# Performance work log

Hardware: AMD Instinct MI355X
Metric: run time of the kernel (lower is better)

Reference implementation:

```python
import jax, jax.numpy as jnp
import numpy as np

WINDOW = 5  # window_size from init
C_COARSE = 256
C_FINE = 128


def _gather_windows(fine_nchw, b, lin_idx, stride, pad, w, wc):
    """Extract [M, w*w, C] windows centered on coarse grid cells.

    Equivalent to F.unfold(kernel=w, stride=stride, padding=pad) followed by
    rearrange('n (c ww) l -> n l ww c') and fancy-indexing [b, lin_idx],
    but gathers only the matched windows.
    """
    x = jnp.pad(fine_nchw, ((0, 0), (0, 0), (pad, pad), (pad, pad)))
    x = jnp.transpose(x, (0, 2, 3, 1))  # [N, Hp, Wp, C]
    r = lin_idx // wc
    c = lin_idx % wc
    offs = jnp.arange(w)
    rows = r[:, None] * stride + offs  # [M, w] (start = r*stride - pad, +pad shift)
    cols = c[:, None] * stride + offs  # [M, w]
    patches = x[b[:, None, None], rows[:, :, None], cols[:, None, :]]  # [M, w, w, C]
    return patches.reshape(patches.shape[0], w * w, patches.shape[-1])


def setup_inputs() -> dict:
    key = jax.random.key(0)
    ks = jax.random.split(key, 10)
    N, Hc, Hf, M = 2, 60, 240, 3000
    inp = {
        "coarse_image_feature_1": jax.random.normal(ks[0], (N, Hc * Hc, C_COARSE), jnp.float32),
        "coarse_image_feature_2": jax.random.normal(ks[1], (N, Hc * Hc, C_COARSE), jnp.float32),
        "fine_image_feature_1": jax.random.normal(ks[2], (N, C_FINE, Hf, Hf), jnp.float32),
        "fine_image_feature_2": jax.random.normal(ks[3], (N, C_FINE, Hf, Hf), jnp.float32),
        "batch_indices": jax.random.randint(ks[4], (M,), 0, N),
        "row_indices": jax.random.randint(ks[5], (M,), 0, Hc * Hc),
        "column_indices": jax.random.randint(ks[6], (M,), 0, Hc * Hc),
        "fine_height_width": Hf,
        "coarse_height_width": Hc,
        # learned params (kaiming-normal-ish weights, zero biases)
        "W_dp": jax.random.normal(ks[7], (C_FINE, C_COARSE), jnp.float32) * np.sqrt(2.0 / C_FINE),
        "b_dp": jnp.zeros((C_FINE,), jnp.float32),
        "W_merge": jax.random.normal(ks[8], (C_FINE, 2 * C_FINE), jnp.float32) * np.sqrt(2.0 / C_FINE),
        "b_merge": jnp.zeros((C_FINE,), jnp.float32),
    }
    return inp


def reference(coarse_image_feature_1, coarse_image_feature_2,
              fine_image_feature_1, fine_image_feature_2,
              batch_indices, row_indices, column_indices,
              fine_height_width, coarse_height_width,
              W_dp, b_dp, W_merge, b_merge):
    stride = fine_height_width // coarse_height_width
    pad = WINDOW // 2
    M = batch_indices.shape[0]

    f1 = _gather_windows(fine_image_feature_1, batch_indices, row_indices,
                         stride, pad, WINDOW, coarse_height_width)       # [M, ww, Cf]
    f2 = _gather_windows(fine_image_feature_2, batch_indices, column_indices,
                         stride, pad, WINDOW, coarse_height_width)       # [M, ww, Cf]

    coarse = jnp.concatenate([
        coarse_image_feature_1[batch_indices, row_indices],
        coarse_image_feature_2[batch_indices, column_indices],
    ], axis=0)                                                           # [2M, Cc]
    coarse = coarse @ W_dp.T + b_dp                                      # [2M, Cf]

    fine = jnp.concatenate([f1, f2], axis=0)                             # [2M, ww, Cf]
    combined = jnp.concatenate(
        [fine, jnp.broadcast_to(coarse[:, None, :], fine.shape)], axis=-1)  # [2M, ww, 2Cf]
    merged = combined @ W_merge.T + b_merge                              # [2M, ww, Cf]
    return merged[:M], merged[M:]
```

## Files before the change

### kernel.cpp

```cpp
#include <hip/hip_runtime.h>

#define HF 240
#define HC 60
#define STRIDEF 4
#define PADW 2
#define WIN 5
#define CC 256
#define CF 128
#define NPOS 25
#define NPX (HF*HF)
#define MPB 16

typedef __bf16 bf16x8 __attribute__((ext_vector_type(8)));
typedef __bf16 bf16x4 __attribute__((ext_vector_type(4)));
typedef float  f32x4  __attribute__((ext_vector_type(4)));

__global__ void k_prep(const float* __restrict__ W_dp, const float* __restrict__ b_dp,
                       const float* __restrict__ W_merge, const float* __restrict__ b_merge,
                       __bf16* __restrict__ Wm1h, float* __restrict__ W_effT,
                       float* __restrict__ b_eff) {
    const int j = blockIdx.x;
    const int k = threadIdx.x;
    const float* wm2 = W_merge + (size_t)j * (2 * CF) + CF;

    float acc = 0.f, accb = 0.f;
    for (int q = 0; q < CF; ++q) {
        const float wq = wm2[q];
        acc  += wq * W_dp[(size_t)q * CC + k];
        accb += wq * b_dp[q];
    }
    W_effT[(size_t)k * CF + j] = acc;

    if (k < CF)
        Wm1h[(size_t)j * CF + k] = (__bf16)W_merge[(size_t)j * (2 * CF) + k];
    if (k == 0)
        b_eff[j] = accb + b_merge[j];
}

__global__ void k_coarse(const float* __restrict__ c1, const float* __restrict__ c2,
                         const int* __restrict__ bidx, const int* __restrict__ ridx,
                         const int* __restrict__ cidx, int M,
                         const float* __restrict__ W_effT, const float* __restrict__ b_eff,
                         float* __restrict__ c_all) {
    const int m0 = blockIdx.x * MPB;
    const int j  = threadIdx.x;
    const int twoM = 2 * M;
    __shared__ float v[MPB * CC];

    const int nm = (twoM - m0) < MPB ? (twoM - m0) : MPB;
    for (int mm = 0; mm < nm; ++mm) {
        int m = m0 + mm;
        const float* src;
        if (m < M) src = c1 + ((size_t)bidx[m] * (HC * HC) + ridx[m]) * CC;
        else       src = c2 + ((size_t)bidx[m - M] * (HC * HC) + cidx[m - M]) * CC;
        v[mm * CC + j]      = src[j];
        v[mm * CC + j + CF] = src[j + CF];
    }
    __syncthreads();

    float acc[MPB];
    const float be = b_eff[j];
    #pragma unroll
    for (int mm = 0; mm < MPB; ++mm) acc[mm] = be;

    for (int k = 0; k < CC; k += 4) {
        float w0 = W_effT[(k + 0) * CF + j];
        float w1 = W_effT[(k + 1) * CF + j];
        float w2 = W_effT[(k + 2) * CF + j];
        float w3 = W_effT[(k + 3) * CF + j];
        #pragma unroll
        for (int mm = 0; mm < MPB; ++mm) {
            const f32x4 vv = *(const f32x4*)&v[mm * CC + k];
            acc[mm] += w0 * vv.x + w1 * vv.y + w2 * vv.z + w3 * vv.w;
        }
    }
    for (int mm = 0; mm < nm; ++mm)
        c_all[(size_t)(m0 + mm) * CF + j] = acc[mm];
}

__global__ __launch_bounds__(256) void k_transpose(
    const float* __restrict__ f1, const float* __restrict__ f2,
    __bf16* __restrict__ T) {
    const int slot = blockIdx.y;
    const float* src = (slot >= 2 ? f2 : f1) + (size_t)(slot & 1) * CF * NPX;
    const int px0 = blockIdx.x * 64;
    const int t = threadIdx.x;

    __shared__ __bf16 tile[64 * CF];

    const int px_l  = t & 63;
    const int chseg = t >> 6;
    const int sw = (px_l & 15) << 3;
    const float* colp = src + px0 + px_l;
    #pragma unroll
    for (int q = 0; q < 8; ++q) {
        const int ch0 = chseg * 32 + q * 4;
        const float v0 = colp[(size_t)(ch0 + 0) * NPX];
        const float v1 = colp[(size_t)(ch0 + 1) * NPX];
        const float v2 = colp[(size_t)(ch0 + 2) * NPX];
        const float v3 = colp[(size_t)(ch0 + 3) * NPX];
        bf16x4 pk = { (__bf16)v0, (__bf16)v1, (__bf16)v2, (__bf16)v3 };
        *(bf16x4*)&tile[px_l * CF + (ch0 ^ sw)] = pk;
    }
    __syncthreads();

    const int l = t & 63;
    const int w = t >> 6;
    __bf16* dst = T + ((size_t)slot * NPX + px0) * CF;
    #pragma unroll
    for (int i = 0; i < 4; ++i) {
        const int pr  = w * 16 + i * 4 + (l >> 4);
        const int ch0 = (l & 15) * 8;
        const bf16x8 vv = *(const bf16x8*)&tile[pr * CF + (ch0 ^ ((pr & 15) << 3))];
        *(bf16x8*)&dst[(size_t)pr * CF + ch0] = vv;
    }
}

__global__ __launch_bounds__(256) void k_main(
    const __bf16* __restrict__ T,
    const int* __restrict__ bidx, const int* __restrict__ ridx,
    const int* __restrict__ cidx, int M,
    const __bf16* __restrict__ Wm1h, const float* __restrict__ c_all,
    float* __restrict__ out) {

    const int m = blockIdx.x;
    const int t = threadIdx.x;
    const int l    = t & 63;
    const int wv   = t >> 6;
    const int lo16 = l & 15;
    const int hi   = l >> 4;

    __shared__ uint patchU[32 * 64];
    __bf16* patch = (__bf16*)patchU;

    int b, lin, ii;
    if (m < M) { ii = 0; b = bidx[m];     lin = ridx[m]; }
    else       { ii = 1; b = bidx[m - M]; lin = cidx[m - M]; }
    const int slot = ii * 2 + b;
    const int r  = lin / HC, c = lin - r * HC;
    const int y0 = r * STRIDEF - PADW;
    const int x0 = c * STRIDEF - PADW;

    bf16x8 bfrag[2][4];
    #pragma unroll
    for (int nt2 = 0; nt2 < 2; ++nt2) {
        const int j = wv * 32 + nt2 * 16 + lo16;
        #pragma unroll
        for (int kt = 0; kt < 4; ++kt)
            bfrag[nt2][kt] = *reinterpret_cast<const bf16x8*>(Wm1h + (size_t)j * CF + kt * 32 + hi * 8);
    }

    const uint* Tb32 = (const uint*)(T + (size_t)slot * NPX * CF);
    for (int p = wv; p < NPOS; p += 4) {
        const int wy = p / WIN, wx = p - wy * WIN;
        const int y = y0 + wy, x = x0 + wx;
        uint v = 0;
        if (y >= 0 && x >= 0)
            v = Tb32[(size_t)(y * HF + x) * (CF / 2) + l];
        patchU[p * 64 + (l ^ ((p & 7) << 2))] = v;
    }
    __syncthreads();

    f32x4 acc[2][2];
    #pragma unroll
    for (int mt = 0; mt < 2; ++mt)
        #pragma unroll
        for (int nt2 = 0; nt2 < 2; ++nt2)
            acc[mt][nt2] = (f32x4){0.f, 0.f, 0.f, 0.f};

    const int swz = (lo16 & 7) << 3;
    #pragma unroll
    for (int kt = 0; kt < 4; ++kt) {
        const int koff = (kt * 32 + hi * 8) ^ swz;
        bf16x8 a0 = *reinterpret_cast<const bf16x8*>(&patch[ lo16       * CF + koff]);
        bf16x8 a1 = *reinterpret_cast<const bf16x8*>(&patch[(16 + lo16) * CF + koff]);
        #pragma unroll
        for (int nt2 = 0; nt2 < 2; ++nt2) {
            acc[0][nt2] = __builtin_amdgcn_mfma_f32_16x16x32_bf16(a0, bfrag[nt2][kt], acc[0][nt2], 0, 0, 0);
            acc[1][nt2] = __builtin_amdgcn_mfma_f32_16x16x32_bf16(a1, bfrag[nt2][kt], acc[1][nt2], 0, 0, 0);
        }
    }

    float* ob = out + (size_t)m * (NPOS * CF);
    #pragma unroll
    for (int nt2 = 0; nt2 < 2; ++nt2) {
        const int j  = wv * 32 + nt2 * 16 + lo16;
        const float cv = c_all[(size_t)m * CF + j];
        #pragma unroll
        for (int mt = 0; mt < 2; ++mt) {
            #pragma unroll
            for (int reg = 0; reg < 4; ++reg) {
                const int p = mt * 16 + hi * 4 + reg;
                if (p < NPOS)
                    ob[(size_t)p * CF + j] = acc[mt][nt2][reg] + cv;
            }
        }
    }
}

__global__ __launch_bounds__(256) void k_main_direct(
    const float* __restrict__ f1, const float* __restrict__ f2,
    const int* __restrict__ bidx, const int* __restrict__ ridx,
    const int* __restrict__ cidx, int M,
    const __bf16* __restrict__ Wm1h, const float* __restrict__ c_all,
    float* __restrict__ out) {

    const int m = blockIdx.x;
    const int t = threadIdx.x;
    const int l    = t & 63;
    const int wv   = t >> 6;
    const int lo16 = l & 15;
    const int hi   = l >> 4;

    __shared__ __bf16 patch[32 * CF];

    bf16x8 bfrag[2][4];
    #pragma unroll
    for (int nt2 = 0; nt2 < 2; ++nt2) {
        const int j = wv * 32 + nt2 * 16 + lo16;
        #pragma unroll
        for (int kt = 0; kt < 4; ++kt)
            bfrag[nt2][kt] = *reinterpret_cast<const bf16x8*>(Wm1h + (size_t)j * CF + kt * 32 + hi * 8);
    }

    const float* img; int b, lin;
    if (m < M) { img = f1; b = bidx[m];     lin = ridx[m]; }
    else       { img = f2; b = bidx[m - M]; lin = cidx[m - M]; }
    const int r  = lin / HC, c = lin - r * HC;
    const int y0 = r * STRIDEF - PADW;
    const int x0 = c * STRIDEF - PADW;

    for (int task = t; task < CF * WIN; task += 256) {
        const int ch = task / WIN;
        const int wy = task - ch * WIN;
        const int y  = y0 + wy;
        const bool yok = (y >= 0);
        const float* rowp = img + (((size_t)b * CF + ch) * HF + (yok ? y : 0)) * HF;
        #pragma unroll
        for (int wx = 0; wx < WIN; ++wx) {
            const int x = x0 + wx;
            const float val = (yok && x >= 0) ? rowp[x] : 0.f;
            const int pos = wy * WIN + wx;
            patch[pos * CF + (ch ^ ((pos & 7) << 3))] = (__bf16)val;
        }
    }
    __syncthreads();

    f32x4 acc[2][2];
    #pragma unroll
    for (int mt = 0; mt < 2; ++mt)
        #pragma unroll
        for (int nt2 = 0; nt2 < 2; ++nt2)
            acc[mt][nt2] = (f32x4){0.f, 0.f, 0.f, 0.f};

    const int swz = (lo16 & 7) << 3;
    #pragma unroll
    for (int kt = 0; kt < 4; ++kt) {
        const int koff = (kt * 32 + hi * 8) ^ swz;
        bf16x8 a0 = *reinterpret_cast<const bf16x8*>(&patch[ lo16       * CF + koff]);
        bf16x8 a1 = *reinterpret_cast<const bf16x8*>(&patch[(16 + lo16) * CF + koff]);
        #pragma unroll
        for (int nt2 = 0; nt2 < 2; ++nt2) {
            acc[0][nt2] = __builtin_amdgcn_mfma_f32_16x16x32_bf16(a0, bfrag[nt2][kt], acc[0][nt2], 0, 0, 0);
            acc[1][nt2] = __builtin_amdgcn_mfma_f32_16x16x32_bf16(a1, bfrag[nt2][kt], acc[1][nt2], 0, 0, 0);
        }
    }

    float* ob = out + (size_t)m * (NPOS * CF);
    #pragma unroll
    for (int nt2 = 0; nt2 < 2; ++nt2) {
        const int j  = wv * 32 + nt2 * 16 + lo16;
        const float cv = c_all[(size_t)m * CF + j];
        #pragma unroll
        for (int mt = 0; mt < 2; ++mt) {
            #pragma unroll
            for (int reg = 0; reg < 4; ++reg) {
                const int p = mt * 16 + hi * 4 + reg;
                if (p < NPOS)
                    ob[(size_t)p * CF + j] = acc[mt][nt2][reg] + cv;
            }
        }
    }
}

extern "C" void kernel_launch(void* const* d_in, const int* in_sizes, int n_in,
                              void* d_out, int out_size, void* d_ws, size_t ws_size,
                              hipStream_t stream) {
    const float* c1      = (const float*)d_in[0];
    const float* c2      = (const float*)d_in[1];
    const float* f1      = (const float*)d_in[2];
    const float* f2      = (const float*)d_in[3];
    const int*   bidx    = (const int*)d_in[4];
    const int*   ridx    = (const int*)d_in[5];
    const int*   cidx    = (const int*)d_in[6];
    const float* W_dp    = (const float*)d_in[9];
    const float* b_dp    = (const float*)d_in[10];
    const float* W_merge = (const float*)d_in[11];
    const float* b_merge = (const float*)d_in[12];
    const int M = in_sizes[4];

    char* ws = (char*)d_ws;
    __bf16* Wm1h  = (__bf16*)(ws);
    float* W_effT = (float*)(ws + (64 << 10));
    float* b_eff  = (float*)(ws + (192 << 10));
    float* c_all  = (float*)(ws + (256 << 10));
    __bf16* T     = (__bf16*)(ws + (4 << 20));

    const size_t need_T = (size_t)(4 << 20) + (size_t)4 * NPX * CF * 2;

    hipLaunchKernelGGL(k_prep, dim3(CF), dim3(CC), 0, stream,
                       W_dp, b_dp, W_merge, b_merge, Wm1h, W_effT, b_eff);

    if (ws_size >= need_T) {
        hipLaunchKernelGGL(k_transpose, dim3(NPX / 64, 4), dim3(256), 0, stream,
                           f1, f2, T);
        hipLaunchKernelGGL(k_coarse, dim3((2 * M + MPB - 1) / MPB), dim3(CF), 0, stream,
                           c1, c2, bidx, ridx, cidx, M, W_effT, b_eff, c_all);
        hipLaunchKernelGGL(k_main, dim3(2 * M), dim3(256), 0, stream,
                           T, bidx, ridx, cidx, M, Wm1h, c_all, (float*)d_out);
    } else {
        hipLaunchKernelGGL(k_coarse, dim3((2 * M + MPB - 1) / MPB), dim3(CF), 0, stream,
                           c1, c2, bidx, ridx, cidx, M, W_effT, b_eff, c_all);
        hipLaunchKernelGGL(k_main_direct, dim3(2 * M), dim3(256), 0, stream,
                           f1, f2, bidx, ridx, cidx, M, Wm1h, c_all, (float*)d_out);
    }
}
```

Measured before the change: 110.5 us.

## Apply merge GEMM to every fine pixel before gathering windows

Instead of gathering 25-pixel windows per match and running the W_merge fine-half GEMM per window, the transpose kernel now multiplies every fine pixel by W_merge once and stores the bf16 result. A light gather kernel then adds the coarse term to each looked-up pixel. Fine pixels are shared across overlapping windows (6000 windows × 25 ≈ 150k lookups versus 230k pixels), so the GEMM work is not clearly reduced. The transposed intermediate keeps the same size and is written once either way. The outputs become bf16-rounded after the GEMM, which adds a small precision difference.

```diff
diff --git a/kernel.cpp b/kernel.cpp
--- a/kernel.cpp
+++ b/kernel.cpp
@@ -10,6 +10,7 @@
 #define NPOS 25
 #define NPX (HF*HF)
 #define MPB 16
+#define PXT 64
 
 typedef __bf16 bf16x8 __attribute__((ext_vector_type(8)));
 typedef __bf16 bf16x4 __attribute__((ext_vector_type(4)));
@@ -78,60 +79,90 @@
         c_all[(size_t)(m0 + mm) * CF + j] = acc[mm];
 }
 
-__global__ __launch_bounds__(256) void k_transpose(
+__global__ __launch_bounds__(256) void k_tgemm(
     const float* __restrict__ f1, const float* __restrict__ f2,
-    __bf16* __restrict__ T) {
+    const __bf16* __restrict__ Wm1h, __bf16* __restrict__ V) {
+
     const int slot = blockIdx.y;
     const float* src = (slot >= 2 ? f2 : f1) + (size_t)(slot & 1) * CF * NPX;
-    const int px0 = blockIdx.x * 64;
-    const int t = threadIdx.x;
-
-    __shared__ __bf16 tile[64 * CF];
-
-    const int px_l  = t & 63;
-    const int chseg = t >> 6;
-    const int sw = (px_l & 15) << 3;
-    const float* colp = src + px0 + px_l;
+    const int px0 = blockIdx.x * PXT;
+    const int t  = threadIdx.x;
+    const int l  = t & 63;
+    const int w  = t >> 6;
+    const int lo16 = l & 15;
+    const int hi   = l >> 4;
+
+    __shared__ __bf16 patch[PXT * CF];
+
+    bf16x8 bfrag[2][4];
+    #pragma unroll
+    for (int nt2 = 0; nt2 < 2; ++nt2) {
+        const int j = w * 32 + nt2 * 16 + lo16;
+        #pragma unroll
+        for (int kt = 0; kt < 4; ++kt)
+            bfrag[nt2][kt] = *reinterpret_cast<const bf16x8*>(Wm1h + (size_t)j * CF + kt * 32 + hi * 8);
+    }
+
+    const int pxl = 4 * lo16;
+    const int sw  = lo16 << 3;
     #pragma unroll
     for (int q = 0; q < 8; ++q) {
-        const int ch0 = chseg * 32 + q * 4;
-        const float v0 = colp[(size_t)(ch0 + 0) * NPX];
-        const float v1 = colp[(size_t)(ch0 + 1) * NPX];
-        const float v2 = colp[(size_t)(ch0 + 2) * NPX];
-        const float v3 = colp[(size_t)(ch0 + 3) * NPX];
-        bf16x4 pk = { (__bf16)v0, (__bf16)v1, (__bf16)v2, (__bf16)v3 };
-        *(bf16x4*)&tile[px_l * CF + (ch0 ^ sw)] = pk;
+        const int ch = w * 32 + q * 4 + hi;
+        const f32x4 vv = *reinterpret_cast<const f32x4*>(src + (size_t)ch * NPX + px0 + pxl);
+        const int chs = ch ^ sw;
+        patch[(pxl + 0) * CF + chs] = (__bf16)vv.x;
+        patch[(pxl + 1) * CF + chs] = (__bf16)vv.y;
+        patch[(pxl + 2) * CF + chs] = (__bf16)vv.z;
+        patch[(pxl + 3) * CF + chs] = (__bf16)vv.w;
     }
     __syncthreads();
 
-    const int l = t & 63;
-    const int w = t >> 6;
-    __bf16* dst = T + ((size_t)slot * NPX + px0) * CF;
-    #pragma unroll
-    for (int i = 0; i < 4; ++i) {
-        const int pr  = w * 16 + i * 4 + (l >> 4);
-        const int ch0 = (l & 15) * 8;
-        const bf16x8 vv = *(const bf16x8*)&tile[pr * CF + (ch0 ^ ((pr & 15) << 3))];
-        *(bf16x8*)&dst[(size_t)pr * CF + ch0] = vv;
-    }
-}
-
-__global__ __launch_bounds__(256) void k_main(
-    const __bf16* __restrict__ T,
+    f32x4 acc[4][2];
+    #pragma unroll
+    for (int mt = 0; mt < 4; ++mt)
+        #pragma unroll
+        for (int nt2 = 0; nt2 < 2; ++nt2)
+            acc[mt][nt2] = (f32x4){0.f, 0.f, 0.f, 0.f};
+
+    #pragma unroll
+    for (int kt = 0; kt < 4; ++kt) {
+        const int k0 = kt * 32 + hi * 8;
+        #pragma unroll
+        for (int mt = 0; mt < 4; ++mt) {
+            const int px = mt * 16 + lo16;
+            const int koff = k0 ^ ((px >> 2) << 3);
+            bf16x8 a = *reinterpret_cast<const bf16x8*>(&patch[px * CF + koff]);
+            #pragma unroll
+            for (int nt2 = 0; nt2 < 2; ++nt2)
+                acc[mt][nt2] = __builtin_amdgcn_mfma_f32_16x16x32_bf16(a, bfrag[nt2][kt], acc[mt][nt2], 0, 0, 0);
+        }
+    }
+
+    __bf16* Vp = V + ((size_t)slot * NPX + px0) * CF;
+    #pragma unroll
+    for (int mt = 0; mt < 4; ++mt) {
+        #pragma unroll
+        for (int nt2 = 0; nt2 < 2; ++nt2) {
+            const int j = w * 32 + nt2 * 16 + lo16;
+            #pragma unroll
+            for (int reg = 0; reg < 4; ++reg) {
+                const int px = mt * 16 + hi * 4 + reg;
+                Vp[(size_t)px * CF + j] = (__bf16)acc[mt][nt2][reg];
+            }
+        }
+    }
+}
+
+__global__ __launch_bounds__(256) void k_gather(
+    const __bf16* __restrict__ V,
     const int* __restrict__ bidx, const int* __restrict__ ridx,
     const int* __restrict__ cidx, int M,
-    const __bf16* __restrict__ Wm1h, const float* __restrict__ c_all,
-    float* __restrict__ out) {
+    const float* __restrict__ c_all, float* __restrict__ out) {
 
     const int m = blockIdx.x;
     const int t = threadIdx.x;
-    const int l    = t & 63;
-    const int wv   = t >> 6;
-    const int lo16 = l & 15;
-    const int hi   = l >> 4;
-
-    __shared__ uint patchU[32 * 64];
-    __bf16* patch = (__bf16*)patchU;
+    const int g  = t >> 5;
+    const int l32 = t & 31;
 
     int b, lin, ii;
     if (m < M) { ii = 0; b = bidx[m];     lin = ridx[m]; }
@@ -141,59 +172,23 @@
     const int y0 = r * STRIDEF - PADW;
     const int x0 = c * STRIDEF - PADW;
 
-    bf16x8 bfrag[2][4];
-    #pragma unroll
-    for (int nt2 = 0; nt2 < 2; ++nt2) {
-        const int j = wv * 32 + nt2 * 16 + lo16;
-        #pragma unroll
-        for (int kt = 0; kt < 4; ++kt)
-            bfrag[nt2][kt] = *reinterpret_cast<const bf16x8*>(Wm1h + (size_t)j * CF + kt * 32 + hi * 8);
-    }
-
-    const uint* Tb32 = (const uint*)(T + (size_t)slot * NPX * CF);
-    for (int p = wv; p < NPOS; p += 4) {
-        const int wy = p / WIN, wx = p - wy * WIN;
-        const int y = y0 + wy, x = x0 + wx;
-        uint v = 0;
-        if (y >= 0 && x >= 0)
-            v = Tb32[(size_t)(y * HF + x) * (CF / 2) + l];
-        patchU[p * 64 + (l ^ ((p & 7) << 2))] = v;
-    }
-    __syncthreads();
-
-    f32x4 acc[2][2];
-    #pragma unroll
-    for (int mt = 0; mt < 2; ++mt)
-        #pragma unroll
-        for (int nt2 = 0; nt2 < 2; ++nt2)
-            acc[mt][nt2] = (f32x4){0.f, 0.f, 0.f, 0.f};
-
-    const int swz = (lo16 & 7) << 3;
-    #pragma unroll
-    for (int kt = 0; kt < 4; ++kt) {
-        const int koff = (kt * 32 + hi * 8) ^ swz;
-        bf16x8 a0 = *reinterpret_cast<const bf16x8*>(&patch[ lo16       * CF + koff]);
-        bf16x8 a1 = *reinterpret_cast<const bf16x8*>(&patch[(16 + lo16) * CF + koff]);
-        #pragma unroll
-        for (int nt2 = 0; nt2 < 2; ++nt2) {
-            acc[0][nt2] = __builtin_amdgcn_mfma_f32_16x16x32_bf16(a0, bfrag[nt2][kt], acc[0][nt2], 0, 0, 0);
-            acc[1][nt2] = __builtin_amdgcn_mfma_f32_16x16x32_bf16(a1, bfrag[nt2][kt], acc[1][nt2], 0, 0, 0);
-        }
-    }
-
-    float* ob = out + (size_t)m * (NPOS * CF);
-    #pragma unroll
-    for (int nt2 = 0; nt2 < 2; ++nt2) {
-        const int j  = wv * 32 + nt2 * 16 + lo16;
-        const float cv = c_all[(size_t)m * CF + j];
-        #pragma unroll
-        for (int mt = 0; mt < 2; ++mt) {
-            #pragma unroll
-            for (int reg = 0; reg < 4; ++reg) {
-                const int p = mt * 16 + hi * 4 + reg;
-                if (p < NPOS)
-                    ob[(size_t)p * CF + j] = acc[mt][nt2][reg] + cv;
+    const f32x4 c4 = *reinterpret_cast<const f32x4*>(c_all + (size_t)m * CF + l32 * 4);
+    const __bf16* Vb = V + (size_t)slot * NPX * CF;
+    float* ob = out + (size_t)m * (NPOS * CF) + l32 * 4;
+
+    #pragma unroll
+    for (int pass = 0; pass < 4; ++pass) {
+        const int p = pass * 8 + g;
+        if (p < NPOS) {
+            const int wy = (p * 13) >> 6;
+            const int wx = p - wy * WIN;
+            const int y = y0 + wy, x = x0 + wx;
+            f32x4 o = c4;
+            if (y >= 0 && x >= 0) {
+                const bf16x4 v = *reinterpret_cast<const bf16x4*>(Vb + (size_t)(y * HF + x) * CF + l32 * 4);
+                o.x += (float)v.x; o.y += (float)v.y; o.z += (float)v.z; o.w += (float)v.w;
             }
+            *reinterpret_cast<f32x4*>(ob + (size_t)p * CF) = o;
         }
     }
 }
@@ -304,23 +299,21 @@
     float* W_effT = (float*)(ws + (64 << 10));
     float* b_eff  = (float*)(ws + (192 << 10));
     float* c_all  = (float*)(ws + (256 << 10));
-    __bf16* T     = (__bf16*)(ws + (4 << 20));
-
-    const size_t need_T = (size_t)(4 << 20) + (size_t)4 * NPX * CF * 2;
+    __bf16* V     = (__bf16*)(ws + (4 << 20));
+
+    const size_t need_V = (size_t)(4 << 20) + (size_t)4 * NPX * CF * 2;
 
     hipLaunchKernelGGL(k_prep, dim3(CF), dim3(CC), 0, stream,
                        W_dp, b_dp, W_merge, b_merge, Wm1h, W_effT, b_eff);
-
-    if (ws_size >= need_T) {
-        hipLaunchKernelGGL(k_transpose, dim3(NPX / 64, 4), dim3(256), 0, stream,
-                           f1, f2, T);
-        hipLaunchKernelGGL(k_coarse, dim3((2 * M + MPB - 1) / MPB), dim3(CF), 0, stream,
-                           c1, c2, bidx, ridx, cidx, M, W_effT, b_eff, c_all);
-        hipLaunchKernelGGL(k_main, dim3(2 * M), dim3(256), 0, stream,
-                           T, bidx, ridx, cidx, M, Wm1h, c_all, (float*)d_out);
+    hipLaunchKernelGGL(k_coarse, dim3((2 * M + MPB - 1) / MPB), dim3(CF), 0, stream,
+                       c1, c2, bidx, ridx, cidx, M, W_effT, b_eff, c_all);
+
+    if (ws_size >= need_V) {
+        hipLaunchKernelGGL(k_tgemm, dim3(NPX / PXT, 4), dim3(256), 0, stream,
+                           f1, f2, Wm1h, V);
+        hipLaunchKernelGGL(k_gather, dim3(2 * M), dim3(256), 0, stream,
+                           V, bidx, ridx, cidx, M, c_all, (float*)d_out);
     } else {
-        hipLaunchKernelGGL(k_coarse, dim3((2 * M + MPB - 1) / MPB), dim3(CF), 0, stream,
-                           c1, c2, bidx, ridx, cidx, M, W_effT, b_eff, c_all);
         hipLaunchKernelGGL(k_main_direct, dim3(2 * M), dim3(256), 0, stream,
                            f1, f2, bidx, ridx, cidx, M, Wm1h, c_all, (float*)d_out);
     }
```

After: 99.45 us. 1.11x faster.
